# Kernel tuning notes

Measured on AMD Instinct MI355X. Metric: run time of the kernel, lower is better.

The kernel has to match this reference:

```python
import jax, jax.numpy as jnp
import numpy as np

EPS = 1e-12  # matches torch F.normalize default eps


def setup_inputs() -> dict:
    key = jax.random.key(0)
    k_x, k_w1, k_b1, k_w2, k_b2 = jax.random.split(key, 5)
    b, n, r, d = 8, 64, 256, 512
    return {
        "x": jax.random.normal(k_x, (b, n, r, d), dtype=jnp.float32),
        "W1": jax.random.normal(k_w1, (d, d), dtype=jnp.float32) * (1.0 / np.sqrt(d)),
        "b1": jax.random.normal(k_b1, (d,), dtype=jnp.float32) * 0.01,
        "W2": jax.random.normal(k_w2, (1, d), dtype=jnp.float32) * (1.0 / np.sqrt(d)),
        "b2": jax.random.normal(k_b2, (1,), dtype=jnp.float32) * 0.01,
    }


def reference(x, W1, b1, W2, b2):
    # F.normalize(x, dim=-1): x / max(||x||_2, eps)
    norm = jnp.sqrt(jnp.sum(x * x, axis=-1, keepdims=True))
    xn = x / jnp.maximum(norm, EPS)                      # [b,n,r,d]
    h = jnp.tanh(jnp.einsum('bnrd,ed->bnre', xn, W1) + b1)  # linear1 + tanh
    scores = (jnp.einsum('bnrd,od->bnro', h, W2) + b2)[..., 0]  # [b,n,r]
    alphas = jax.nn.softmax(scores, axis=2)              # softmax over regions r
    fbar = jnp.einsum('bnr,bnrd->bnd', alphas, xn)       # weighted pooling
    return (fbar, alphas)
```

## Files before the change

### kernel.cpp

```cpp
#include <hip/hip_runtime.h>
#include <hip/hip_bf16.h>

typedef short short8 __attribute__((ext_vector_type(8)));
typedef float floatx4 __attribute__((ext_vector_type(4)));

#define NGROUP 512
#define RREG 256
#define D 512
#define ROWS 131072
#define FBAR_ELEMS (NGROUP * D)

__device__ __forceinline__ unsigned short f2bf(float f) {
    unsigned int u = __float_as_uint(f);
    unsigned int r = (u + 0x7fffu + ((u >> 16) & 1u)) >> 16;
    return (unsigned short)r;
}
__device__ __forceinline__ float fast_tanh(float x) {
    float cx = fminf(fmaxf(x, -9.5f), 9.5f);
    float e  = __builtin_amdgcn_exp2f(cx * 2.8853900817779268f);
    return (e - 1.f) * __builtin_amdgcn_rcpf(e + 1.f);
}

__global__ __launch_bounds__(256) void conv_w1(const float* __restrict__ W1,
                                               unsigned short* __restrict__ W1c) {
    int tid = blockIdx.x * 256 + threadIdx.x;
    int P = tid * 8;
    int kc = P >> 15;
    int L = P & 32767;
    int col = L >> 6;
    int q = L & 63;
    int kl = (q ^ ((col & 3) << 4)) >> 1;
    const float* src = W1 + col * 512 + kc * 32 + kl;
    float4 v = *reinterpret_cast<const float4*>(src);
    ushort4 o;
    o.x = f2bf(v.x); o.y = f2bf(v.y); o.z = f2bf(v.z); o.w = f2bf(v.w);
    *reinterpret_cast<ushort4*>((char*)W1c + P) = o;
}

__global__ __launch_bounds__(512) void score_gemm(
    const float* __restrict__ x, const unsigned short* __restrict__ W1c,
    const float* __restrict__ b1, const float* __restrict__ W2v,
    float* __restrict__ inv_norm, float* __restrict__ scores) {

    __shared__ unsigned short A_lds[32768];
    __shared__ char B_lds[3][8][4096];

    const int t = threadIdx.x;
    const int lane = t & 63;
    const int w = t >> 6;
    const int cl = lane & 15;
    const int hi = lane >> 4;
    const size_t row0 = (size_t)blockIdx.x * 64;

    auto stageB = [&](int buf, int kc) {
        const char* gb = (const char*)W1c + kc * 32768 + w * 4096 + lane * 16;
        char* lb = &B_lds[buf][w][0];
        #pragma unroll
        for (int i = 0; i < 4; ++i) {
            __builtin_amdgcn_global_load_lds(
                (const __attribute__((address_space(1))) void*)(gb + i * 1024),
                (__attribute__((address_space(3))) void*)(lb + i * 1024),
                16, 0, 0);
        }
    };

    stageB(0, 0);
    stageB(1, 1);

    {
        const float* xw = x + (row0 + w * 8) * (size_t)D + lane * 8;
        float4 v[8][2];
        #pragma unroll
        for (int i = 0; i < 8; ++i) {
            v[i][0] = *reinterpret_cast<const float4*>(xw + (size_t)i * D);
            v[i][1] = *reinterpret_cast<const float4*>(xw + (size_t)i * D + 4);
        }
        #pragma unroll
        for (int i = 0; i < 8; ++i) {
            int r = w * 8 + i;
            float4 p = v[i][0], q = v[i][1];
            float ss = p.x*p.x + p.y*p.y + p.z*p.z + p.w*p.w
                     + q.x*q.x + q.y*q.y + q.z*q.z + q.w*q.w;
            #pragma unroll
            for (int m = 1; m < 64; m <<= 1) ss += __shfl_xor(ss, m, 64);
            float inv = 1.0f / fmaxf(sqrtf(ss), 1e-12f);
            if (lane == 0) inv_norm[row0 + r] = inv;
            short8 pk;
            pk[0] = (short)f2bf(p.x); pk[1] = (short)f2bf(p.y);
            pk[2] = (short)f2bf(p.z); pk[3] = (short)f2bf(p.w);
            pk[4] = (short)f2bf(q.x); pk[5] = (short)f2bf(q.y);
            pk[6] = (short)f2bf(q.z); pk[7] = (short)f2bf(q.w);
            *reinterpret_cast<short8*>(
                (char*)A_lds + r * 1024 + ((lane * 16) ^ ((r & 7) << 4))) = pk;
        }
    }
    __syncthreads();

    floatx4 acc[4][4];
    #pragma unroll
    for (int tt = 0; tt < 4; ++tt)
        #pragma unroll
        for (int f = 0; f < 4; ++f) acc[tt][f] = floatx4{0, 0, 0, 0};

    const int aswz = (cl & 7) << 4;
    const int bofs = (hi * 16) ^ ((cl & 3) << 4);

    #pragma unroll
    for (int s = 0; s < 16; ++s) {
        if (s <= 13) {
            stageB((s + 2) % 3, s + 2);
            asm volatile("s_waitcnt vmcnt(8)" ::: "memory");
        } else if (s == 14) {
            asm volatile("s_waitcnt vmcnt(4)" ::: "memory");
        } else {
            asm volatile("s_waitcnt vmcnt(0)" ::: "memory");
        }

        const char* Bb = &B_lds[s % 3][w][0];
        short8 bfr[4], afr[4];
        #pragma unroll
        for (int f = 0; f < 4; ++f)
            bfr[f] = *reinterpret_cast<const short8*>(Bb + (f * 16 + cl) * 64 + bofs);
        #pragma unroll
        for (int tt = 0; tt < 4; ++tt)
            afr[tt] = *reinterpret_cast<const short8*>(
                (char*)A_lds + (tt * 16 + cl) * 1024 + ((s * 64 + hi * 16) ^ aswz));

        #pragma unroll
        for (int tt = 0; tt < 4; ++tt)
            #pragma unroll
            for (int f = 0; f < 4; ++f)
                acc[tt][f] = __builtin_amdgcn_mfma_f32_16x16x32_bf16(
                    afr[tt], bfr[f], acc[tt][f], 0, 0, 0);
    }

    float sp[4][4];
    #pragma unroll
    for (int tt = 0; tt < 4; ++tt)
        #pragma unroll
        for (int i = 0; i < 4; ++i) sp[tt][i] = 0.f;

    float4 iv4[4];
    #pragma unroll
    for (int tt = 0; tt < 4; ++tt)
        iv4[tt] = *reinterpret_cast<const float4*>(inv_norm + row0 + tt * 16 + hi * 4);

    #pragma unroll
    for (int f = 0; f < 4; ++f) {
        int col = w * 64 + f * 16 + cl;
        float wv = W2v[col];
        float bb = b1[col];
        #pragma unroll
        for (int tt = 0; tt < 4; ++tt) {
            sp[tt][0] += wv * fast_tanh(acc[tt][f][0] * iv4[tt].x + bb);
            sp[tt][1] += wv * fast_tanh(acc[tt][f][1] * iv4[tt].y + bb);
            sp[tt][2] += wv * fast_tanh(acc[tt][f][2] * iv4[tt].z + bb);
            sp[tt][3] += wv * fast_tanh(acc[tt][f][3] * iv4[tt].w + bb);
        }
    }

    float red[4][4];
    #pragma unroll
    for (int tt = 0; tt < 4; ++tt) {
        #pragma unroll
        for (int i = 0; i < 4; ++i) {
            float v = sp[tt][i];
            v += __shfl_xor(v, 1, 64);
            v += __shfl_xor(v, 2, 64);
            v += __shfl_xor(v, 4, 64);
            v += __shfl_xor(v, 8, 64);
            red[tt][i] = v;
        }
    }

    __syncthreads();
    float* scorebuf = (float*)A_lds;
    if (cl == 0) {
        #pragma unroll
        for (int tt = 0; tt < 4; ++tt)
            #pragma unroll
            for (int i = 0; i < 4; ++i)
                scorebuf[w * 64 + tt * 16 + hi * 4 + i] = red[tt][i];
    }
    __syncthreads();

    if (t < 64) {
        float s = 0.f;
        #pragma unroll
        for (int q = 0; q < 8; ++q) s += scorebuf[q * 64 + t];
        scores[row0 + t] = s;
    }
}

__global__ __launch_bounds__(512) void softmax_pool(
    const float* __restrict__ x, const float* __restrict__ inv_norm,
    const float* __restrict__ scores, float* __restrict__ out) {

    __shared__ float F[RREG];
    __shared__ float wts[RREG];
    const int t = threadIdx.x;
    const int g = blockIdx.x;

    float s = 0.f, e = 0.f;
    if (t < RREG) { s = scores[g * RREG + t]; F[t] = s; }
    __syncthreads();
    for (int off = 128; off > 0; off >>= 1) {
        if (t < off) F[t] = fmaxf(F[t], F[t + off]);
        __syncthreads();
    }
    float mx = F[0];
    __syncthreads();
    if (t < RREG) { e = expf(s - mx); F[t] = e; }
    __syncthreads();
    for (int off = 128; off > 0; off >>= 1) {
        if (t < off) F[t] += F[t + off];
        __syncthreads();
    }
    float denom = F[0];
    if (t < RREG) {
        float al = e / denom;
        out[FBAR_ELEMS + (size_t)g * RREG + t] = al;
        wts[t] = al * inv_norm[(size_t)g * RREG + t];
    }
    __syncthreads();

    float a = 0.f;
    const float* xb = x + (size_t)g * RREG * D + t;
    #pragma unroll 16
    for (int r = 0; r < RREG; ++r) a += wts[r] * xb[(size_t)r * D];
    out[(size_t)g * D + t] = a;
}

extern "C" void kernel_launch(void* const* d_in, const int* in_sizes, int n_in,
                              void* d_out, int out_size, void* d_ws, size_t ws_size,
                              hipStream_t stream) {
    const float* x  = (const float*)d_in[0];
    const float* W1 = (const float*)d_in[1];
    const float* b1 = (const float*)d_in[2];
    const float* w2 = (const float*)d_in[3];
    float* out = (float*)d_out;

    unsigned short* W1c = (unsigned short*)d_ws;
    float* inv_norm = (float*)((char*)d_ws + 524288);
    float* scores   = (float*)((char*)d_ws + 1048576);

    conv_w1<<<256, 256, 0, stream>>>(W1, W1c);
    score_gemm<<<ROWS / 64, 512, 0, stream>>>(x, W1c, b1, w2, inv_norm, scores);
    softmax_pool<<<NGROUP, 512, 0, stream>>>(x, inv_norm, scores, out);
}
```

Before: 185.3 us.

## Make score GEMM persistent over four row tiles with prefetched x loads

Measured after the change: 205.0 us. 1.11x slower.

```diff
diff --git a/kernel.cpp b/kernel.cpp
--- a/kernel.cpp
+++ b/kernel.cpp
@@ -9,6 +9,9 @@
 #define D 512
 #define ROWS 131072
 #define FBAR_ELEMS (NGROUP * D)
+#define TROWS 64
+#define NTILE 4
+#define GRID (ROWS / (TROWS * NTILE))
 
 __device__ __forceinline__ unsigned short f2bf(float f) {
     unsigned int u = __float_as_uint(f);
@@ -37,20 +40,21 @@
     *reinterpret_cast<ushort4*>((char*)W1c + P) = o;
 }
 
-__global__ __launch_bounds__(512) void score_gemm(
+__global__ __launch_bounds__(512, 1) void score_gemm(
     const float* __restrict__ x, const unsigned short* __restrict__ W1c,
     const float* __restrict__ b1, const float* __restrict__ W2v,
-    float* __restrict__ inv_norm, float* __restrict__ scores) {
-
-    __shared__ unsigned short A_lds[32768];
-    __shared__ char B_lds[3][8][4096];
+    float* __restrict__ inv_norm, float* __restrict__ scorespart) {
+
+    __shared__ unsigned short A_lds[TROWS * 512];
+    __shared__ char B_lds[2][8][4096];
+    __shared__ float inv_s[TROWS];
 
     const int t = threadIdx.x;
     const int lane = t & 63;
     const int w = t >> 6;
     const int cl = lane & 15;
     const int hi = lane >> 4;
-    const size_t row0 = (size_t)blockIdx.x * 64;
+    const size_t brow0 = (size_t)blockIdx.x * (TROWS * NTILE);
 
     auto stageB = [&](int buf, int kc) {
         const char* gb = (const char*)W1c + kc * 32768 + w * 4096 + lane * 16;
@@ -64,137 +68,146 @@
         }
     };
 
-    stageB(0, 0);
-    stageB(1, 1);
-
-    {
-        const float* xw = x + (row0 + w * 8) * (size_t)D + lane * 8;
-        float4 v[8][2];
-        #pragma unroll
-        for (int i = 0; i < 8; ++i) {
-            v[i][0] = *reinterpret_cast<const float4*>(xw + (size_t)i * D);
-            v[i][1] = *reinterpret_cast<const float4*>(xw + (size_t)i * D + 4);
-        }
-        #pragma unroll
-        for (int i = 0; i < 8; ++i) {
-            int r = w * 8 + i;
-            float4 p = v[i][0], q = v[i][1];
-            float ss = p.x*p.x + p.y*p.y + p.z*p.z + p.w*p.w
-                     + q.x*q.x + q.y*q.y + q.z*q.z + q.w*q.w;
-            #pragma unroll
-            for (int m = 1; m < 64; m <<= 1) ss += __shfl_xor(ss, m, 64);
-            float inv = 1.0f / fmaxf(sqrtf(ss), 1e-12f);
-            if (lane == 0) inv_norm[row0 + r] = inv;
+    const int pr = t >> 3;
+    const int c0 = (t & 7) * 64;
+    float4 xv[16];
+
+    auto loadX = [&](size_t trow0) {
+        const float* xb = x + (trow0 + pr) * (size_t)D + c0;
+        #pragma unroll
+        for (int j = 0; j < 16; ++j)
+            xv[j] = *reinterpret_cast<const float4*>(xb + j * 4);
+    };
+    auto packA = [&](size_t trow0) {
+        float ss = 0.f;
+        #pragma unroll
+        for (int j = 0; j < 16; ++j)
+            ss += xv[j].x*xv[j].x + xv[j].y*xv[j].y + xv[j].z*xv[j].z + xv[j].w*xv[j].w;
+        ss += __shfl_xor(ss, 1, 8);
+        ss += __shfl_xor(ss, 2, 8);
+        ss += __shfl_xor(ss, 4, 8);
+        float inv = 1.0f / fmaxf(sqrtf(ss), 1e-12f);
+        if ((t & 7) == 0) { inv_s[pr] = inv; inv_norm[trow0 + pr] = inv; }
+        const int swz = (pr & 7) << 4;
+        #pragma unroll
+        for (int q = 0; q < 8; ++q) {
+            float4 p = xv[2 * q], r = xv[2 * q + 1];
             short8 pk;
             pk[0] = (short)f2bf(p.x); pk[1] = (short)f2bf(p.y);
             pk[2] = (short)f2bf(p.z); pk[3] = (short)f2bf(p.w);
-            pk[4] = (short)f2bf(q.x); pk[5] = (short)f2bf(q.y);
-            pk[6] = (short)f2bf(q.z); pk[7] = (short)f2bf(q.w);
+            pk[4] = (short)f2bf(r.x); pk[5] = (short)f2bf(r.y);
+            pk[6] = (short)f2bf(r.z); pk[7] = (short)f2bf(r.w);
             *reinterpret_cast<short8*>(
-                (char*)A_lds + r * 1024 + ((lane * 16) ^ ((r & 7) << 4))) = pk;
-        }
-    }
-    __syncthreads();
-
-    floatx4 acc[4][4];
-    #pragma unroll
-    for (int tt = 0; tt < 4; ++tt)
-        #pragma unroll
-        for (int f = 0; f < 4; ++f) acc[tt][f] = floatx4{0, 0, 0, 0};
+                (char*)A_lds + pr * 1024 + (((t & 7) * 128 + q * 16) ^ swz)) = pk;
+        }
+    };
+
+    stageB(0, 0);
+    stageB(1, 1);
+    loadX(brow0);
+    packA(brow0);
+    __syncthreads();
 
     const int aswz = (cl & 7) << 4;
     const int bofs = (hi * 16) ^ ((cl & 3) << 4);
 
-    #pragma unroll
-    for (int s = 0; s < 16; ++s) {
-        if (s <= 13) {
-            stageB((s + 2) % 3, s + 2);
-            asm volatile("s_waitcnt vmcnt(8)" ::: "memory");
-        } else if (s == 14) {
-            asm volatile("s_waitcnt vmcnt(4)" ::: "memory");
-        } else {
-            asm volatile("s_waitcnt vmcnt(0)" ::: "memory");
-        }
-
-        const char* Bb = &B_lds[s % 3][w][0];
-        short8 bfr[4], afr[4];
-        #pragma unroll
-        for (int f = 0; f < 4; ++f)
-            bfr[f] = *reinterpret_cast<const short8*>(Bb + (f * 16 + cl) * 64 + bofs);
+    for (int tile = 0; tile < NTILE; ++tile) {
+        const size_t trow0 = brow0 + (size_t)tile * TROWS;
+
+        floatx4 acc[4][4];
         #pragma unroll
         for (int tt = 0; tt < 4; ++tt)
-            afr[tt] = *reinterpret_cast<const short8*>(
-                (char*)A_lds + (tt * 16 + cl) * 1024 + ((s * 64 + hi * 16) ^ aswz));
-
-        #pragma unroll
-        for (int tt = 0; tt < 4; ++tt)
+            #pragma unroll
+            for (int f = 0; f < 4; ++f) acc[tt][f] = floatx4{0, 0, 0, 0};
+
+        #pragma unroll 4
+        for (int s = 0; s < 16; ++s) {
+            if (s < 15) {
+                stageB((s + 1) & 1, s + 1);
+                asm volatile("s_waitcnt vmcnt(4)" ::: "memory");
+            } else {
+                asm volatile("s_waitcnt vmcnt(0)" ::: "memory");
+            }
+            const char* Bb = &B_lds[s & 1][w][0];
+            short8 bfr[4], afr[4];
             #pragma unroll
             for (int f = 0; f < 4; ++f)
-                acc[tt][f] = __builtin_amdgcn_mfma_f32_16x16x32_bf16(
-                    afr[tt], bfr[f], acc[tt][f], 0, 0, 0);
-    }
-
-    float sp[4][4];
-    #pragma unroll
-    for (int tt = 0; tt < 4; ++tt)
-        #pragma unroll
-        for (int i = 0; i < 4; ++i) sp[tt][i] = 0.f;
-
-    float4 iv4[4];
-    #pragma unroll
-    for (int tt = 0; tt < 4; ++tt)
-        iv4[tt] = *reinterpret_cast<const float4*>(inv_norm + row0 + tt * 16 + hi * 4);
-
-    #pragma unroll
-    for (int f = 0; f < 4; ++f) {
-        int col = w * 64 + f * 16 + cl;
-        float wv = W2v[col];
-        float bb = b1[col];
+                bfr[f] = *reinterpret_cast<const short8*>(Bb + (f * 16 + cl) * 64 + bofs);
+            #pragma unroll
+            for (int tt = 0; tt < 4; ++tt)
+                afr[tt] = *reinterpret_cast<const short8*>(
+                    (char*)A_lds + (tt * 16 + cl) * 1024 + ((s * 64 + hi * 16) ^ aswz));
+            #pragma unroll
+            for (int tt = 0; tt < 4; ++tt)
+                #pragma unroll
+                for (int f = 0; f < 4; ++f)
+                    acc[tt][f] = __builtin_amdgcn_mfma_f32_16x16x32_bf16(
+                        afr[tt], bfr[f], acc[tt][f], 0, 0, 0);
+        }
+
+        if (tile < NTILE - 1) { stageB(0, 0); stageB(1, 1); }
+
+        float sp[4][4];
+        float4 iv4[4];
         #pragma unroll
         for (int tt = 0; tt < 4; ++tt) {
-            sp[tt][0] += wv * fast_tanh(acc[tt][f][0] * iv4[tt].x + bb);
-            sp[tt][1] += wv * fast_tanh(acc[tt][f][1] * iv4[tt].y + bb);
-            sp[tt][2] += wv * fast_tanh(acc[tt][f][2] * iv4[tt].z + bb);
-            sp[tt][3] += wv * fast_tanh(acc[tt][f][3] * iv4[tt].w + bb);
-        }
-    }
-
-    float red[4][4];
-    #pragma unroll
-    for (int tt = 0; tt < 4; ++tt) {
-        #pragma unroll
-        for (int i = 0; i < 4; ++i) {
-            float v = sp[tt][i];
-            v += __shfl_xor(v, 1, 64);
-            v += __shfl_xor(v, 2, 64);
-            v += __shfl_xor(v, 4, 64);
-            v += __shfl_xor(v, 8, 64);
-            red[tt][i] = v;
-        }
-    }
-
-    __syncthreads();
-    float* scorebuf = (float*)A_lds;
-    if (cl == 0) {
-        #pragma unroll
-        for (int tt = 0; tt < 4; ++tt)
-            #pragma unroll
-            for (int i = 0; i < 4; ++i)
-                scorebuf[w * 64 + tt * 16 + hi * 4 + i] = red[tt][i];
-    }
-    __syncthreads();
-
-    if (t < 64) {
-        float s = 0.f;
-        #pragma unroll
-        for (int q = 0; q < 8; ++q) s += scorebuf[q * 64 + t];
-        scores[row0 + t] = s;
+            iv4[tt] = *reinterpret_cast<const float4*>(&inv_s[tt * 16 + hi * 4]);
+            #pragma unroll
+            for (int i = 0; i < 4; ++i) sp[tt][i] = 0.f;
+        }
+        #pragma unroll
+        for (int f = 0; f < 4; ++f) {
+            int col = w * 64 + f * 16 + cl;
+            float wv = W2v[col];
+            float bb = b1[col];
+            #pragma unroll
+            for (int tt = 0; tt < 2; ++tt) {
+                sp[tt][0] += wv * fast_tanh(acc[tt][f][0] * iv4[tt].x + bb);
+                sp[tt][1] += wv * fast_tanh(acc[tt][f][1] * iv4[tt].y + bb);
+                sp[tt][2] += wv * fast_tanh(acc[tt][f][2] * iv4[tt].z + bb);
+                sp[tt][3] += wv * fast_tanh(acc[tt][f][3] * iv4[tt].w + bb);
+            }
+        }
+
+        if (tile < NTILE - 1) loadX(trow0 + TROWS);
+
+        #pragma unroll
+        for (int f = 0; f < 4; ++f) {
+            int col = w * 64 + f * 16 + cl;
+            float wv = W2v[col];
+            float bb = b1[col];
+            #pragma unroll
+            for (int tt = 2; tt < 4; ++tt) {
+                sp[tt][0] += wv * fast_tanh(acc[tt][f][0] * iv4[tt].x + bb);
+                sp[tt][1] += wv * fast_tanh(acc[tt][f][1] * iv4[tt].y + bb);
+                sp[tt][2] += wv * fast_tanh(acc[tt][f][2] * iv4[tt].z + bb);
+                sp[tt][3] += wv * fast_tanh(acc[tt][f][3] * iv4[tt].w + bb);
+            }
+        }
+
+        #pragma unroll
+        for (int tt = 0; tt < 4; ++tt) {
+            #pragma unroll
+            for (int i = 0; i < 4; ++i) {
+                float v = sp[tt][i];
+                v += __shfl_xor(v, 1, 64);
+                v += __shfl_xor(v, 2, 64);
+                v += __shfl_xor(v, 4, 64);
+                v += __shfl_xor(v, 8, 64);
+                if (cl == 0)
+                    scorespart[(size_t)w * ROWS + trow0 + tt * 16 + hi * 4 + i] = v;
+            }
+        }
+
+        __syncthreads();
+        if (tile < NTILE - 1) packA(trow0 + TROWS);
+        __syncthreads();
     }
 }
 
 __global__ __launch_bounds__(512) void softmax_pool(
     const float* __restrict__ x, const float* __restrict__ inv_norm,
-    const float* __restrict__ scores, float* __restrict__ out) {
+    const float* __restrict__ scorespart, float* __restrict__ out) {
 
     __shared__ float F[RREG];
     __shared__ float wts[RREG];
@@ -202,7 +215,12 @@
     const int g = blockIdx.x;
 
     float s = 0.f, e = 0.f;
-    if (t < RREG) { s = scores[g * RREG + t]; F[t] = s; }
+    if (t < RREG) {
+        #pragma unroll
+        for (int q = 0; q < 8; ++q)
+            s += scorespart[(size_t)q * ROWS + (size_t)g * RREG + t];
+        F[t] = s;
+    }
     __syncthreads();
     for (int off = 128; off > 0; off >>= 1) {
         if (t < off) F[t] = fmaxf(F[t], F[t + off]);
@@ -240,11 +258,11 @@
     const float* w2 = (const float*)d_in[3];
     float* out = (float*)d_out;
 
-    unsigned short* W1c = (unsigned short*)d_ws;
-    float* inv_norm = (float*)((char*)d_ws + 524288);
-    float* scores   = (float*)((char*)d_ws + 1048576);
+    unsigned short* W1c  = (unsigned short*)d_ws;
+    float* inv_norm      = (float*)((char*)d_ws + 524288);
+    float* scorespart    = (float*)((char*)d_ws + 1048576);
 
     conv_w1<<<256, 256, 0, stream>>>(W1, W1c);
-    score_gemm<<<ROWS / 64, 512, 0, stream>>>(x, W1c, b1, w2, inv_norm, scores);
-    softmax_pool<<<NGROUP, 512, 0, stream>>>(x, inv_norm, scores, out);
-}
+    score_gemm<<<GRID, 512, 0, stream>>>(x, W1c, b1, w2, inv_norm, scorespart);
+    softmax_pool<<<NGROUP, 512, 0, stream>>>(x, inv_norm, scorespart, out);
+}
```
